# Kernel tuning notes

Hardware: AMD Instinct MI355X
Metric: run time of the kernel (lower is better)

The kernel has to match this reference:

```python
import jax, jax.numpy as jnp
import numpy as np

L, B, S, H = 2, 32, 2048, 512


def setup_inputs() -> dict:
    key = jax.random.key(0)
    k0, k1, k2, k3, k4 = jax.random.split(key, 5)
    scale = 1.0 / np.sqrt(H).astype(np.float32)  # ~PyTorch LSTMCell init scale
    return {
        "X": jax.random.normal(k0, (B, S, H), jnp.float32),
        "W_ih": jax.random.normal(k1, (L, 4 * H, H), jnp.float32) * scale,
        "W_hh": jax.random.normal(k2, (L, 4 * H, H), jnp.float32) * scale,
        "b_ih": jax.random.normal(k3, (L, 4 * H), jnp.float32) * scale,
        "b_hh": jax.random.normal(k4, (L, 4 * H), jnp.float32) * scale,
    }


def _lstm_layer(x, Wih, Whh, bih, bhh):
    # x: [S, B, I]; gate order matches torch.nn.LSTMCell: i, f, g, o
    Bb = x.shape[1]
    Hh = Whh.shape[1]
    h0 = jnp.zeros((Bb, Hh), x.dtype)
    c0 = jnp.zeros((Bb, Hh), x.dtype)
    # precompute input contribution for all timesteps: [S, B, 4H]
    xg = jnp.einsum('sbi,gi->sbg', x, Wih) + bih + bhh

    def step(carry, xg_t):
        h, c = carry
        gates = xg_t + h @ Whh.T  # [B, 4H]
        i, f, g, o = jnp.split(gates, 4, axis=-1)
        c = jax.nn.sigmoid(f) * c + jax.nn.sigmoid(i) * jnp.tanh(g)
        h = jax.nn.sigmoid(o) * jnp.tanh(c)
        return (h, c), h

    (hT, cT), hs = jax.lax.scan(step, (h0, c0), xg)
    return hs, hT, cT  # hs: [S, B, H]


def reference(X, W_ih, W_hh, b_ih, b_hh):
    # eval mode: variational dropout (dropout_i = dropout_h = 0) is identity;
    # no residual, no reverse.
    x = jnp.transpose(X, (1, 0, 2))  # [S, B, I]
    n_layers = W_ih.shape[0]
    hT = cT = None
    for l in range(n_layers):
        x, hT, cT = _lstm_layer(x, W_ih[l], W_hh[l], b_ih[l], b_hh[l])
    ht = jnp.transpose(x, (1, 0, 2))  # [B, S, H]
    # states = (ht[:, -1], ct[:, -1]) of final layer
    return ht, hT, cT
```

## Files before the change

### kernel.cpp

```cpp
#include <hip/hip_runtime.h>

typedef unsigned short u16;
typedef unsigned int u32;
typedef unsigned long long u64;
typedef __attribute__((ext_vector_type(4))) float f32x4;
typedef __attribute__((ext_vector_type(8))) short bf16x8;

#define S_LEN 2048
#define BATCH 32
#define HID 512
#define NG 2048
#define NWG 64
#define SLICE 8

#define MFMA16(a, b, c) __builtin_amdgcn_mfma_f32_16x16x32_bf16((a), (b), (c), 0, 0, 0)

__device__ __forceinline__ u16 f2bf(float f) {
  u32 u = __builtin_bit_cast(u32, f);
  u32 r = (u + 0x7FFFu + ((u >> 16) & 1u)) >> 16;
  return (u16)r;
}
__device__ __forceinline__ float bf2f(u16 u) {
  u32 x = ((u32)u) << 16;
  return __builtin_bit_cast(float, x);
}
__device__ __forceinline__ float sigf(float x) {
  return 1.0f / (1.0f + __expf(-x));
}
__device__ __forceinline__ float tanh_fast(float x) {
  float a = fabsf(x);
  float t = __expf(-2.0f * a);
  float r = (1.0f - t) / (1.0f + t);
  return x < 0.0f ? -r : r;
}

__device__ __forceinline__ uint4 bypass_ld16(const u16* p) {
  uint4 r;
  asm volatile("global_load_dwordx4 %0, %1, off sc0 sc1"
               : "=v"(r) : "v"(p) : "memory");
  return r;
}
__device__ __forceinline__ void bypass_wait() {
  asm volatile("s_waitcnt vmcnt(0)" ::: "memory");
  __builtin_amdgcn_sched_barrier(0);
}

__global__ void prep_weights(const float* __restrict__ Wih, const float* __restrict__ Whh,
                             const float* __restrict__ bih, const float* __restrict__ bhh,
                             u16* __restrict__ wih_bf, u16* __restrict__ whh_bf,
                             float* __restrict__ bsum) {
  const int i = blockIdx.x * 256 + threadIdx.x;
  wih_bf[i] = f2bf(Wih[i]);
  whh_bf[i] = f2bf(Whh[i]);
  if (i < 2 * NG) bsum[i] = bih[i] + bhh[i];
}

__global__ __launch_bounds__(256)
void gemm_xg(const float* __restrict__ Ap, const u16* __restrict__ Bw,
             const float* __restrict__ bias, void* __restrict__ xgp, int xg32)
{
  __shared__ __align__(16) u16 aT[64][72];
  __shared__ __align__(16) u16 bT[64][72];
  const int tid = threadIdx.x;
  const int nb = blockIdx.x;
  const int mb = blockIdx.y;
  const int lane = tid & 63, wid = tid >> 6;
  const int mw = (wid & 1) * 32, nw = (wid >> 1) * 32;
  f32x4 acc[2][2] = {{{0.f,0.f,0.f,0.f},{0.f,0.f,0.f,0.f}},
                     {{0.f,0.f,0.f,0.f},{0.f,0.f,0.f,0.f}}};

  const int arow = tid >> 2;
  const int gm = mb * 64 + arow;
  const int t = gm >> 5, b = gm & 31;
  const size_t aoff = ((size_t)b * S_LEN + t) * HID;
  const size_t boff = (size_t)(nb * 64 + arow) * HID;
  const int c16 = (tid & 3) * 16;

  for (int kb = 0; kb < 8; ++kb) {
    const int k0 = kb * 64;
    {
      const float* src = Ap + aoff + k0 + c16;
      #pragma unroll
      for (int q = 0; q < 4; ++q) {
        const float4 v = ((const float4*)src)[q];
        ushort4 w4;
        w4.x = f2bf(v.x); w4.y = f2bf(v.y); w4.z = f2bf(v.z); w4.w = f2bf(v.w);
        *(ushort4*)&aT[arow][c16 + q * 4] = w4;
      }
    }
    {
      const uint4* src = (const uint4*)(Bw + boff + k0 + c16);
      const uint4 v0 = src[0], v1 = src[1];
      *(uint4*)&bT[arow][c16] = v0;
      *(uint4*)&bT[arow][c16 + 8] = v1;
    }
    __syncthreads();
    #pragma unroll
    for (int kk = 0; kk < 2; ++kk) {
      const int ko = kk * 32 + (lane >> 4) * 8;
      const bf16x8 a0 = *(const bf16x8*)&aT[mw +      (lane & 15)][ko];
      const bf16x8 a1 = *(const bf16x8*)&aT[mw + 16 + (lane & 15)][ko];
      const bf16x8 b0 = *(const bf16x8*)&bT[nw +      (lane & 15)][ko];
      const bf16x8 b1 = *(const bf16x8*)&bT[nw + 16 + (lane & 15)][ko];
      acc[0][0] = MFMA16(a0, b0, acc[0][0]);
      acc[0][1] = MFMA16(a0, b1, acc[0][1]);
      acc[1][0] = MFMA16(a1, b0, acc[1][0]);
      acc[1][1] = MFMA16(a1, b1, acc[1][1]);
    }
    __syncthreads();
  }
  const int col = lane & 15, rb = (lane >> 4) * 4;
  #pragma unroll
  for (int fm = 0; fm < 2; ++fm) {
    #pragma unroll
    for (int fn = 0; fn < 2; ++fn) {
      const int gn = nb * 64 + nw + fn * 16 + col;
      const float bv = bias[gn];
      #pragma unroll
      for (int r = 0; r < 4; ++r) {
        const size_t gmr = (size_t)(mb * 64 + mw + fm * 16 + rb + r);
        const float v = acc[fm][fn][r] + bv;
        if (xg32) ((float*)xgp)[gmr * NG + gn] = v;
        else      ((u16*)xgp)[gmr * NG + gn] = f2bf(v);
      }
    }
  }
}

__global__ __launch_bounds__(256, 1)
void lstm_fused(const void* __restrict__ xgp, int xg32,
                const u16* __restrict__ whh_bf, const u16* __restrict__ wih_bf,
                const float* __restrict__ bsum,
                u16* __restrict__ hb1, u16* __restrict__ hb2,
                float* __restrict__ dout, u32* __restrict__ flags)
{
  __shared__ __align__(16) u16 wR[32][520];
  __shared__ __align__(16) u16 wI[32][520];
  __shared__ __align__(16) u16 hA[32][520];
  __shared__ __align__(16) u16 hB[32][520];
  __shared__ float gT[32][33];

  const int blk = blockIdx.x;
  const int layer = blk >> 6;
  const int w = blk & 63;
  const int tid = threadIdx.x;
  const int lane = tid & 63, wid = tid >> 6;
  const int mw = (wid & 1) * 16, nw = (wid >> 1) * 16;
  const int b = tid >> 3, j = tid & 7;
  u32* f_l1  = flags;
  u32* f_own = flags + layer * 64;

  const u16* Whh = whh_bf + (size_t)layer * NG * HID;
  #pragma unroll
  for (int i = tid; i < 32 * 64; i += 256) {
    const int r = i >> 6, ch = i & 63;
    const int gnrow = (r >> 3) * HID + w * SLICE + (r & 7);
    *(uint4*)&wR[r][ch * 8] = *(const uint4*)&Whh[(size_t)gnrow * HID + ch * 8];
  }
  float bv[4] = {0.f, 0.f, 0.f, 0.f};
  if (layer == 1) {
    const u16* Wih2 = wih_bf + (size_t)NG * HID;
    #pragma unroll
    for (int i = tid; i < 32 * 64; i += 256) {
      const int r = i >> 6, ch = i & 63;
      const int gnrow = (r >> 3) * HID + w * SLICE + (r & 7);
      *(uint4*)&wI[r][ch * 8] = *(const uint4*)&Wih2[(size_t)gnrow * HID + ch * 8];
    }
    #pragma unroll
    for (int g = 0; g < 4; ++g) bv[g] = bsum[NG + g * HID + w * SLICE + j];
  }
  u16* hb_own = layer ? hb2 : hb1;
  float c = 0.0f;
  __syncthreads();

  for (int t = 0; t < S_LEN; ++t) {
    float xv[4];

    if (layer == 0) {
      if (xg32) {
        const float* x = (const float*)xgp + ((size_t)t * BATCH + b) * NG + w * SLICE + j;
        #pragma unroll
        for (int g = 0; g < 4; ++g) xv[g] = __builtin_nontemporal_load(&x[g * HID]);
      } else {
        const u16* x = (const u16*)xgp + ((size_t)t * BATCH + b) * NG + w * SLICE + j;
        #pragma unroll
        for (int g = 0; g < 4; ++g) xv[g] = bf2f(__builtin_nontemporal_load(&x[g * HID]));
      }
    } else {
      #pragma unroll
      for (int g = 0; g < 4; ++g) xv[g] = bv[g];
    }

    if (layer == 1) {
      if (wid == 0) {
        const u32 tgt = (u32)(t + 1);
        while (true) {
          u32 v = __hip_atomic_load(&f_l1[lane], __ATOMIC_RELAXED,
                                    __HIP_MEMORY_SCOPE_AGENT);
          if (__all((int)(v >= tgt))) break;
          __builtin_amdgcn_s_sleep(1);
        }
      } else if (wid == 1 && t > 0) {
        const u32 tgt = (u32)t;
        while (true) {
          u32 v = __hip_atomic_load(&f_own[lane], __ATOMIC_RELAXED,
                                    __HIP_MEMORY_SCOPE_AGENT);
          if (__all((int)(v >= tgt))) break;
          __builtin_amdgcn_s_sleep(1);
        }
      }
    } else if (t > 0) {
      if (wid == 0) {
        const u32 tgt = (u32)t;
        while (true) {
          u32 v = __hip_atomic_load(&f_own[lane], __ATOMIC_RELAXED,
                                    __HIP_MEMORY_SCOPE_AGENT);
          if (__all((int)(v >= tgt))) break;
          __builtin_amdgcn_s_sleep(1);
        }
      }
    }
    __syncthreads();

    const u16* srcA = nullptr;
    const u16* srcB = nullptr;
    if (layer == 1) {
      srcA = hb1 + (size_t)t * (BATCH * HID);
      if (t > 0) srcB = hb2 + (size_t)(t - 1) * (BATCH * HID);
    } else if (t > 0) {
      srcA = hb1 + (size_t)(t - 1) * (BATCH * HID);
    }
    uint4 vA[8], vB[8];
    if (srcA) {
      #pragma unroll
      for (int ii = 0; ii < 8; ++ii) {
        const int i = tid + ii * 256, r = i >> 6, cc = i & 63;
        vA[ii] = bypass_ld16(srcA + (size_t)r * HID + cc * 8);
      }
    }
    if (srcB) {
      #pragma unroll
      for (int ii = 0; ii < 8; ++ii) {
        const int i = tid + ii * 256, r = i >> 6, cc = i & 63;
        vB[ii] = bypass_ld16(srcB + (size_t)r * HID + cc * 8);
      }
    }
    bypass_wait();
    if (srcA) {
      #pragma unroll
      for (int ii = 0; ii < 8; ++ii) {
        const int i = tid + ii * 256, r = i >> 6, cc = i & 63;
        *(uint4*)&hA[r][cc * 8] = vA[ii];
      }
    }
    if (srcB) {
      #pragma unroll
      for (int ii = 0; ii < 8; ++ii) {
        const int i = tid + ii * 256, r = i >> 6, cc = i & 63;
        *(uint4*)&hB[r][cc * 8] = vB[ii];
      }
    }
    __syncthreads();

    f32x4 ac0 = {0.f,0.f,0.f,0.f}, ac1 = {0.f,0.f,0.f,0.f};
    if (layer == 1) {
      #pragma unroll
      for (int kt = 0; kt < 16; ++kt) {
        const int ko = kt * 32 + (lane >> 4) * 8;
        const bf16x8 a  = *(const bf16x8*)&hA[mw + (lane & 15)][ko];
        const bf16x8 bb = *(const bf16x8*)&wI[nw + (lane & 15)][ko];
        if (kt & 1) ac1 = MFMA16(a, bb, ac1); else ac0 = MFMA16(a, bb, ac0);
      }
      if (t > 0) {
        #pragma unroll
        for (int kt = 0; kt < 16; ++kt) {
          const int ko = kt * 32 + (lane >> 4) * 8;
          const bf16x8 a  = *(const bf16x8*)&hB[mw + (lane & 15)][ko];
          const bf16x8 bb = *(const bf16x8*)&wR[nw + (lane & 15)][ko];
          if (kt & 1) ac1 = MFMA16(a, bb, ac1); else ac0 = MFMA16(a, bb, ac0);
        }
      }
    } else if (t > 0) {
      #pragma unroll
      for (int kt = 0; kt < 16; ++kt) {
        const int ko = kt * 32 + (lane >> 4) * 8;
        const bf16x8 a  = *(const bf16x8*)&hA[mw + (lane & 15)][ko];
        const bf16x8 bb = *(const bf16x8*)&wR[nw + (lane & 15)][ko];
        if (kt & 1) ac1 = MFMA16(a, bb, ac1); else ac0 = MFMA16(a, bb, ac0);
      }
    }
    const f32x4 acc = ac0 + ac1;

    #pragma unroll
    for (int r = 0; r < 4; ++r)
      gT[mw + (lane >> 4) * 4 + r][nw + (lane & 15)] = acc[r];
    __syncthreads();

    float pre[4];
    #pragma unroll
    for (int g = 0; g < 4; ++g) pre[g] = xv[g] + gT[b][g * SLICE + j];

    const float gi = sigf(pre[0]);
    const float gf = sigf(pre[1]);
    const float gg = tanh_fast(pre[2]);
    const float go = sigf(pre[3]);
    c = gf * c + gi * gg;
    const float h = go * tanh_fast(c);

    {
      const u32 me  = (u32)f2bf(h);
      const u32 oth = (u32)__shfl_xor((int)me, 1);
      if ((j & 1) == 0) {
        u32* dst = (u32*)(hb_own + (size_t)t * (BATCH * HID) + b * HID + w * SLICE + j);
        __hip_atomic_store(dst, me | (oth << 16), __ATOMIC_RELAXED,
                           __HIP_MEMORY_SCOPE_AGENT);
      }
    }
    __syncthreads();
    if (tid == 0) {
      __hip_atomic_store(&f_own[w], (u32)(t + 1), __ATOMIC_RELAXED,
                         __HIP_MEMORY_SCOPE_AGENT);
    }
    if (layer == 1) {
      dout[((size_t)b * S_LEN + t) * HID + w * SLICE + j] = h;
      if (t == S_LEN - 1) {
        dout[(size_t)BATCH * S_LEN * HID + b * HID + w * SLICE + j] = h;
        dout[(size_t)BATCH * S_LEN * HID + (size_t)BATCH * HID + b * HID + w * SLICE + j] = c;
      }
    }
  }
}

extern "C" void kernel_launch(void* const* d_in, const int* in_sizes, int n_in,
                              void* d_out, int out_size, void* d_ws, size_t ws_size,
                              hipStream_t stream) {
  (void)in_sizes; (void)n_in; (void)out_size;
  const float* X   = (const float*)d_in[0];
  const float* Wih = (const float*)d_in[1];
  const float* Whh = (const float*)d_in[2];
  const float* bih = (const float*)d_in[3];
  const float* bhh = (const float*)d_in[4];

  const size_t M      = (size_t)S_LEN * BATCH;
  const size_t xg_b32 = M * NG * 4;
  const size_t xg_b16 = M * NG * 2;
  const size_t hb_b   = M * HID * 2;
  const size_t w_b    = 2ull * NG * HID * 2;
  const size_t fixed  = 2 * hb_b + 2 * w_b + 16384 + 1024;

  const int xg32 = (ws_size >= xg_b32 + fixed) ? 1 : 0;

  char* p = (char*)d_ws;
  auto carve = [&](size_t bytes) { char* q = p; p += (bytes + 255) & ~(size_t)255; return q; };
  void* xg     = carve(xg32 ? xg_b32 : xg_b16);
  u16*  hb1    = (u16*)carve(hb_b);
  u16*  hb2    = (u16*)carve(hb_b);
  u16*  wih_bf = (u16*)carve(w_b);
  u16*  whh_bf = (u16*)carve(w_b);
  float* bsum  = (float*)carve(16384);
  u32*  flags  = (u32*)carve(1024);

  hipMemsetAsync(flags, 0, 1024, stream);
  prep_weights<<<(2 * NG * HID) / 256, 256, 0, stream>>>(Wih, Whh, bih, bhh,
                                                         wih_bf, whh_bf, bsum);
  gemm_xg<<<dim3(32, 1024), 256, 0, stream>>>(X, wih_bf, bsum, xg, xg32);
  lstm_fused<<<2 * NWG, 256, 0, stream>>>(xg, xg32, whh_bf, wih_bf, bsum,
                                          hb1, hb2, (float*)d_out, flags);
}
```

Baseline: 8.207 ms.

## Replace per-step flag barriers with sentinel-filled hidden buffers polled directly

Removes the per-timestep flag counters and their spin-waits, and drops the extra __syncthreads plus flag store after writing h. Instead, the hidden-state history buffers are pre-filled with a sentinel bf16 pair (2.0,2.0). Each block spins reloading the needed h rows until no sentinel remains. This cuts one global round-trip and a barrier from the serial recurrence critical path. The risk is false stalls if a real h pair ever equals the sentinel value, plus the cost of filling the full history buffers up front.

Result: faster. 7.892 ms (-3.8%).

```diff
diff --git a/kernel.cpp b/kernel.cpp
--- a/kernel.cpp
+++ b/kernel.cpp
@@ -5,6 +5,7 @@
 typedef unsigned long long u64;
 typedef __attribute__((ext_vector_type(4))) float f32x4;
 typedef __attribute__((ext_vector_type(8))) short bf16x8;
+typedef __attribute__((ext_vector_type(4))) u32 u32x4;
 
 #define S_LEN 2048
 #define BATCH 32
@@ -13,6 +14,8 @@
 #define NWG 64
 #define SLICE 8
 
+#define SENT 0x40004000u
+
 #define MFMA16(a, b, c) __builtin_amdgcn_mfma_f32_16x16x32_bf16((a), (b), (c), 0, 0, 0)
 
 __device__ __forceinline__ u16 f2bf(float f) {
@@ -34,15 +37,27 @@
   return x < 0.0f ? -r : r;
 }
 
-__device__ __forceinline__ uint4 bypass_ld16(const u16* p) {
-  uint4 r;
+__device__ __forceinline__ u32x4 bypass_ld16(const u16* p) {
+  u32x4 r;
   asm volatile("global_load_dwordx4 %0, %1, off sc0 sc1"
                : "=v"(r) : "v"(p) : "memory");
   return r;
 }
+__device__ __forceinline__ void bypass_st16(u16* p, u32x4 v) {
+  asm volatile("global_store_dwordx4 %0, %1, off sc0 sc1"
+               :: "v"(p), "v"(v) : "memory");
+}
 __device__ __forceinline__ void bypass_wait() {
   asm volatile("s_waitcnt vmcnt(0)" ::: "memory");
   __builtin_amdgcn_sched_barrier(0);
+}
+
+__global__ void fill_sentinel(u16* base, int n16) {
+  u32x4 v = {SENT, SENT, SENT, SENT};
+  const int step = gridDim.x * 256;
+  for (int i = blockIdx.x * 256 + threadIdx.x; i < n16; i += step)
+    bypass_st16(base + (size_t)i * 8, v);
+  asm volatile("s_waitcnt vmcnt(0)" ::: "memory");
 }
 
 __global__ void prep_weights(const float* __restrict__ Wih, const float* __restrict__ Whh,
@@ -132,7 +147,7 @@
                 const u16* __restrict__ whh_bf, const u16* __restrict__ wih_bf,
                 const float* __restrict__ bsum,
                 u16* __restrict__ hb1, u16* __restrict__ hb2,
-                float* __restrict__ dout, u32* __restrict__ flags)
+                float* __restrict__ dout)
 {
   __shared__ __align__(16) u16 wR[32][520];
   __shared__ __align__(16) u16 wI[32][520];
@@ -147,8 +162,6 @@
   const int lane = tid & 63, wid = tid >> 6;
   const int mw = (wid & 1) * 16, nw = (wid >> 1) * 16;
   const int b = tid >> 3, j = tid & 7;
-  u32* f_l1  = flags;
-  u32* f_own = flags + layer * 64;
 
   const u16* Whh = whh_bf + (size_t)layer * NG * HID;
   #pragma unroll
@@ -190,37 +203,6 @@
       #pragma unroll
       for (int g = 0; g < 4; ++g) xv[g] = bv[g];
     }
-
-    if (layer == 1) {
-      if (wid == 0) {
-        const u32 tgt = (u32)(t + 1);
-        while (true) {
-          u32 v = __hip_atomic_load(&f_l1[lane], __ATOMIC_RELAXED,
-                                    __HIP_MEMORY_SCOPE_AGENT);
-          if (__all((int)(v >= tgt))) break;
-          __builtin_amdgcn_s_sleep(1);
-        }
-      } else if (wid == 1 && t > 0) {
-        const u32 tgt = (u32)t;
-        while (true) {
-          u32 v = __hip_atomic_load(&f_own[lane], __ATOMIC_RELAXED,
-                                    __HIP_MEMORY_SCOPE_AGENT);
-          if (__all((int)(v >= tgt))) break;
-          __builtin_amdgcn_s_sleep(1);
-        }
-      }
-    } else if (t > 0) {
-      if (wid == 0) {
-        const u32 tgt = (u32)t;
-        while (true) {
-          u32 v = __hip_atomic_load(&f_own[lane], __ATOMIC_RELAXED,
-                                    __HIP_MEMORY_SCOPE_AGENT);
-          if (__all((int)(v >= tgt))) break;
-          __builtin_amdgcn_s_sleep(1);
-        }
-      }
-    }
-    __syncthreads();
 
     const u16* srcA = nullptr;
     const u16* srcB = nullptr;
@@ -230,34 +212,46 @@
     } else if (t > 0) {
       srcA = hb1 + (size_t)(t - 1) * (BATCH * HID);
     }
-    uint4 vA[8], vB[8];
+    u32x4 vA[8], vB[8];
     if (srcA) {
+      while (true) {
+        #pragma unroll
+        for (int ii = 0; ii < 8; ++ii) {
+          const int i = tid + ii * 256, r = i >> 6, cc = i & 63;
+          vA[ii] = bypass_ld16(srcA + (size_t)r * HID + cc * 8);
+        }
+        if (srcB) {
+          #pragma unroll
+          for (int ii = 0; ii < 8; ++ii) {
+            const int i = tid + ii * 256, r = i >> 6, cc = i & 63;
+            vB[ii] = bypass_ld16(srcB + (size_t)r * HID + cc * 8);
+          }
+        }
+        bypass_wait();
+        u32 bad = 0;
+        #pragma unroll
+        for (int ii = 0; ii < 8; ++ii)
+          bad |= (u32)(vA[ii][0] == SENT) | (u32)(vA[ii][1] == SENT) |
+                 (u32)(vA[ii][2] == SENT) | (u32)(vA[ii][3] == SENT);
+        if (srcB) {
+          #pragma unroll
+          for (int ii = 0; ii < 8; ++ii)
+            bad |= (u32)(vB[ii][0] == SENT) | (u32)(vB[ii][1] == SENT) |
+                   (u32)(vB[ii][2] == SENT) | (u32)(vB[ii][3] == SENT);
+        }
+        if (__all((int)(bad == 0))) break;
+      }
       #pragma unroll
       for (int ii = 0; ii < 8; ++ii) {
         const int i = tid + ii * 256, r = i >> 6, cc = i & 63;
-        vA[ii] = bypass_ld16(srcA + (size_t)r * HID + cc * 8);
-      }
-    }
-    if (srcB) {
-      #pragma unroll
-      for (int ii = 0; ii < 8; ++ii) {
-        const int i = tid + ii * 256, r = i >> 6, cc = i & 63;
-        vB[ii] = bypass_ld16(srcB + (size_t)r * HID + cc * 8);
-      }
-    }
-    bypass_wait();
-    if (srcA) {
-      #pragma unroll
-      for (int ii = 0; ii < 8; ++ii) {
-        const int i = tid + ii * 256, r = i >> 6, cc = i & 63;
-        *(uint4*)&hA[r][cc * 8] = vA[ii];
-      }
-    }
-    if (srcB) {
-      #pragma unroll
-      for (int ii = 0; ii < 8; ++ii) {
-        const int i = tid + ii * 256, r = i >> 6, cc = i & 63;
-        *(uint4*)&hB[r][cc * 8] = vB[ii];
+        *(u32x4*)&hA[r][cc * 8] = vA[ii];
+      }
+      if (srcB) {
+        #pragma unroll
+        for (int ii = 0; ii < 8; ++ii) {
+          const int i = tid + ii * 256, r = i >> 6, cc = i & 63;
+          *(u32x4*)&hB[r][cc * 8] = vB[ii];
+        }
       }
     }
     __syncthreads();
@@ -312,14 +306,9 @@
       const u32 oth = (u32)__shfl_xor((int)me, 1);
       if ((j & 1) == 0) {
         u32* dst = (u32*)(hb_own + (size_t)t * (BATCH * HID) + b * HID + w * SLICE + j);
-        __hip_atomic_store(dst, me | (oth << 16), __ATOMIC_RELAXED,
-                           __HIP_MEMORY_SCOPE_AGENT);
-      }
-    }
-    __syncthreads();
-    if (tid == 0) {
-      __hip_atomic_store(&f_own[w], (u32)(t + 1), __ATOMIC_RELAXED,
-                         __HIP_MEMORY_SCOPE_AGENT);
+        asm volatile("global_store_dword %0, %1, off sc0 sc1"
+                     :: "v"(dst), "v"(me | (oth << 16)) : "memory");
+      }
     }
     if (layer == 1) {
       dout[((size_t)b * S_LEN + t) * HID + w * SLICE + j] = h;
@@ -358,12 +347,11 @@
   u16*  wih_bf = (u16*)carve(w_b);
   u16*  whh_bf = (u16*)carve(w_b);
   float* bsum  = (float*)carve(16384);
-  u32*  flags  = (u32*)carve(1024);
-
-  hipMemsetAsync(flags, 0, 1024, stream);
+
+  fill_sentinel<<<2048, 256, 0, stream>>>(hb1, (int)((2 * hb_b) / 16));
   prep_weights<<<(2 * NG * HID) / 256, 256, 0, stream>>>(Wih, Whh, bih, bhh,
                                                          wih_bf, whh_bf, bsum);
   gemm_xg<<<dim3(32, 1024), 256, 0, stream>>>(X, wih_bf, bsum, xg, xg32);
   lstm_fused<<<2 * NWG, 256, 0, stream>>>(xg, xg32, whh_bf, wih_bf, bsum,
-                                          hb1, hb2, (float*)d_out, flags);
-}
+                                          hb1, hb2, (float*)d_out);
+}
```
